# Kernel optimization log

Measured on AMD Instinct MI355X. Metric: run time of the kernel, lower is better.

## Reference

```python
import jax, jax.numpy as jnp
import numpy as np

D_MODEL = 1024
N_HEADS = 32
HEAD_DIM = D_MODEL // N_HEADS
EPS = 1e-5


def setup_inputs() -> dict:
    key = jax.random.key(0)
    ks = jax.random.split(key, 6)
    B, S = 2, 2048
    scale = 1.0 / np.sqrt(D_MODEL)
    return {
        "x": jax.random.normal(ks[0], (B, S, D_MODEL), dtype=jnp.float32),
        "Wqkv_w": jax.random.normal(ks[1], (3 * D_MODEL, D_MODEL), dtype=jnp.float32) * scale,
        "Wqkv_b": jax.random.normal(ks[2], (3 * D_MODEL,), dtype=jnp.float32) * 0.01,
        "gn_w": jnp.ones((D_MODEL,), dtype=jnp.float32),
        "gn_b": jnp.zeros((D_MODEL,), dtype=jnp.float32),
        "out_w": jax.random.normal(ks[3], (D_MODEL, D_MODEL), dtype=jnp.float32) * scale,
        "out_b": jax.random.normal(ks[4], (D_MODEL,), dtype=jnp.float32) * 0.01,
    }


def reference(x, Wqkv_w, Wqkv_b, gn_w, gn_b, out_w, out_b):
    B, S, Dm = x.shape
    H, Dh = N_HEADS, HEAD_DIM
    # QKV projection
    qkv = x @ Wqkv_w.T + Wqkv_b                      # [B,S,3*Dm]
    qkv = qkv.reshape(B, S, 3, H, Dh)
    q, k, v = qkv[:, :, 0], qkv[:, :, 1], qkv[:, :, 2]  # each [B,S,H,Dh]
    # Linear (softmax-free) attention; dropout p=0 -> identity
    a = jnp.einsum('bthd,bshd->bhts', q, k)          # [B,H,S,S]
    ctx = jnp.einsum('bhts,bshd->bthd', a, v)        # [B,S,H,Dh]
    # GroupNorm(num_groups=H, num_channels=Dm) on transposed (B, Dm, S):
    # normalizes jointly over (Dh channels, S positions) per (batch, group)
    g = ctx.transpose(0, 2, 3, 1)                    # [B,H,Dh,S]
    mean = g.mean(axis=(2, 3), keepdims=True)
    var = ((g - mean) ** 2).mean(axis=(2, 3), keepdims=True)
    gh = (g - mean) * jax.lax.rsqrt(var + EPS)
    gh = gh * gn_w.reshape(H, Dh, 1) + gn_b.reshape(H, Dh, 1)
    ctx = gh.transpose(0, 3, 1, 2).reshape(B, S, Dm)  # back to [B,S,Dm]
    return ctx @ out_w.T + out_b
```

## Files before the change

### kernel.cpp

```cpp
#include <hip/hip_runtime.h>
#include <hip/hip_bf16.h>
#include <stdint.h>

typedef unsigned short ushort_t;
typedef __attribute__((ext_vector_type(4))) float f32x4;
typedef __attribute__((ext_vector_type(8))) short short8;

#define SS 2048
#define ROWS 4096
#define EPS 1e-5f

__device__ __forceinline__ unsigned short f2bf(float f) {
  unsigned int u = __float_as_uint(f);
  u += 0x7FFF + ((u >> 16) & 1);
  return (unsigned short)(u >> 16);
}
__device__ __forceinline__ float bf2f(short s) {
  return __uint_as_float(((unsigned int)(unsigned short)s) << 16);
}

#define GLDS16(g, l)                                                        \
  __builtin_amdgcn_global_load_lds((__attribute__((address_space(1))) void*)(g), \
                                   (__attribute__((address_space(3))) void*)(l), 16, 0, 0)

__global__ __launch_bounds__(256) void f2b3_kernel(const float* __restrict__ a,
                                                   ushort_t* __restrict__ oa, int n4a,
                                                   const float* __restrict__ b,
                                                   ushort_t* __restrict__ ob, int n4b,
                                                   const float* __restrict__ c,
                                                   ushort_t* __restrict__ oc, int n4c) {
  const int stride = gridDim.x * blockDim.x;
  const int total = n4a + n4b + n4c;
  for (int i = blockIdx.x * blockDim.x + threadIdx.x; i < total; i += stride) {
    const float* src; ushort_t* dst; int idx;
    if (i < n4a)            { src = a; dst = oa; idx = i; }
    else if (i < n4a + n4b) { src = b; dst = ob; idx = i - n4a; }
    else                    { src = c; dst = oc; idx = i - n4a - n4b; }
    const float4 v = reinterpret_cast<const float4*>(src)[idx];
    ushort4 o;
    o.x = f2bf(v.x); o.y = f2bf(v.y); o.z = f2bf(v.z); o.w = f2bf(v.w);
    reinterpret_cast<ushort4*>(dst)[idx] = o;
  }
}

#define MF(d, va, vb) d = __builtin_amdgcn_mfma_f32_16x16x32_bf16(va, vb, d, 0, 0, 0)
#define LD8(p) (*reinterpret_cast<const short8*>(p))

__global__ __launch_bounds__(512, 2) void gemm1_pipe(const ushort_t* __restrict__ A,
                                                     const ushort_t* __restrict__ B,
                                                     const float* __restrict__ bias,
                                                     ushort_t* __restrict__ C) {
  __shared__ __align__(16) ushort_t lds[4 * 14336];
  const int tid = threadIdx.x;
  const int wid = tid >> 6, lane = tid & 63;
  const int bm = blockIdx.x * 256, bn = blockIdx.y * 192;
  const int wm = wid >> 2, wn = wid & 3;

  const int srow = lane >> 2;
  const int scol = ((lane & 3) ^ ((lane >> 3) & 3)) * 8;
  const int widb = (wid < 6) ? wid : 0;
  const ushort_t* gA0 = A + (size_t)(bm + wid * 16 + srow) * 1024 + scol;
  const ushort_t* gA1 = A + (size_t)(bm + (8 + wid) * 16 + srow) * 1024 + scol;
  const ushort_t* gB0 = B + (size_t)(bn + widb * 16 + srow) * 1024 + scol;
  const ushort_t* gB1 = B + (size_t)(bn + (6 + widb) * 16 + srow) * 1024 + scol;

  const int lf = lane & 15, kf = lane >> 4;
  const int flip = ((lane >> 1) & 3) << 4;
  const int aBase = (((wm * 128 + lf) * 64 + kf * 16) ^ flip) >> 1;
  const int bBase = ((((wn * 48 + lf) * 64 + kf * 16) ^ flip) >> 1) + 8192;

  f32x4 acc[8][3] = {};

#define STAGE_A(t)                                                           \
  { ushort_t* d = lds + (((t) & 3) * 14336);                                 \
    GLDS16(gA0 + (t) * 32, d + wid * 512);                                   \
    GLDS16(gA1 + (t) * 32, d + (8 + wid) * 512); }
#define STAGE_B(t)                                                           \
  if (wid < 6) { ushort_t* d = lds + (((t) & 3) * 14336) + 8192;             \
    GLDS16(gB0 + (t) * 32, d + wid * 512);                                   \
    GLDS16(gB1 + (t) * 32, d + (6 + wid) * 512); }

  STAGE_A(0) STAGE_B(0)
  STAGE_A(1) STAGE_B(1)
  STAGE_A(2) STAGE_B(2)
  if (wid < 6) { asm volatile("s_waitcnt vmcnt(8)" ::: "memory"); }
  else         { asm volatile("s_waitcnt vmcnt(4)" ::: "memory"); }
  __builtin_amdgcn_s_barrier();
  __builtin_amdgcn_sched_barrier(0);

#define K_TILE(t, DO_STAGE, VM6, VM2)                                        \
  { const ushort_t* Lb = lds + (((t) & 3) * 14336);                          \
    short8 bv0 = LD8(Lb + bBase);                                            \
    short8 bv1 = LD8(Lb + bBase + 512);                                      \
    short8 bv2 = LD8(Lb + bBase + 1024);                                     \
    short8 a0 = LD8(Lb + aBase);                                             \
    short8 a1 = LD8(Lb + aBase + 512);                                       \
    short8 a2 = LD8(Lb + aBase + 1024);                                      \
    short8 a3 = LD8(Lb + aBase + 1536);                                      \
    if (DO_STAGE) STAGE_A((t) + 3)                                           \
    __builtin_amdgcn_s_setprio(1);                                           \
    MF(acc[0][0], a0, bv0); MF(acc[1][0], a1, bv0);                          \
    MF(acc[0][1], a0, bv1); MF(acc[1][1], a1, bv1);                          \
    MF(acc[0][2], a0, bv2); MF(acc[1][2], a1, bv2);                          \
    MF(acc[2][0], a2, bv0); MF(acc[3][0], a3, bv0);                          \
    MF(acc[2][1], a2, bv1); MF(acc[3][1], a3, bv1);                          \
    MF(acc[2][2], a2, bv2); MF(acc[3][2], a3, bv2);                          \
    __builtin_amdgcn_s_setprio(0);                                           \
    a0 = LD8(Lb + aBase + 2048);                                             \
    a1 = LD8(Lb + aBase + 2560);                                             \
    a2 = LD8(Lb + aBase + 3072);                                             \
    a3 = LD8(Lb + aBase + 3584);                                             \
    if (DO_STAGE) STAGE_B((t) + 3)                                           \
    __builtin_amdgcn_s_setprio(1);                                           \
    MF(acc[4][0], a0, bv0); MF(acc[5][0], a1, bv0);                          \
    MF(acc[4][1], a0, bv1); MF(acc[5][1], a1, bv1);                          \
    MF(acc[4][2], a0, bv2); MF(acc[5][2], a1, bv2);                          \
    MF(acc[6][0], a2, bv0); MF(acc[7][0], a3, bv0);                          \
    MF(acc[6][1], a2, bv1); MF(acc[7][1], a3, bv1);                          \
    MF(acc[6][2], a2, bv2); MF(acc[7][2], a3, bv2);                          \
    __builtin_amdgcn_s_setprio(0);                                           \
    __builtin_amdgcn_sched_barrier(0);                                       \
    if (wid < 6) { asm volatile("s_waitcnt vmcnt(" #VM6 ")" ::: "memory"); } \
    else         { asm volatile("s_waitcnt vmcnt(" #VM2 ")" ::: "memory"); } \
    __builtin_amdgcn_s_barrier();                                            \
    __builtin_amdgcn_sched_barrier(0); }

#pragma unroll 1
  for (int t = 0; t < 29; ++t) K_TILE(t, 1, 8, 4)
  K_TILE(29, 0, 4, 2)
  K_TILE(30, 0, 0, 0)
  K_TILE(31, 0, 0, 0)

  const int crow = bm + wm * 128 + (lane >> 4) * 4;
  const int ccol = bn + wn * 48 + (lane & 15);
#pragma unroll
  for (int m = 0; m < 8; ++m)
#pragma unroll
    for (int n = 0; n < 3; ++n) {
      const int col = ccol + n * 16;
      const float bb = bias[col];
#pragma unroll
      for (int j = 0; j < 4; ++j)
        C[(size_t)(crow + m * 16 + j) * 3072 + col] = f2bf(acc[m][n][j] + bb);
    }
#undef K_TILE
#undef STAGE_A
#undef STAGE_B
}

__global__ __launch_bounds__(256, 2) void gemm2_pipe(const ushort_t* __restrict__ A,
                                                     const ushort_t* __restrict__ B,
                                                     const float* __restrict__ bias,
                                                     float* __restrict__ C) {
  __shared__ __align__(16) ushort_t lds[4 * 6144];
  const int tid = threadIdx.x;
  const int wid = tid >> 6, lane = tid & 63;
  const int bm = blockIdx.x * 64, bn = blockIdx.y * 128;
  const int wm = wid >> 1, wn = wid & 1;

  const int srow = lane >> 2;
  const int scol = ((lane & 3) ^ ((lane >> 3) & 3)) * 8;
  const ushort_t* gA  = A + (size_t)(bm + wid * 16 + srow) * 1024 + scol;
  const ushort_t* gB0 = B + (size_t)(bn + wid * 16 + srow) * 1024 + scol;
  const ushort_t* gB1 = B + (size_t)(bn + (4 + wid) * 16 + srow) * 1024 + scol;

  const int lf = lane & 15, kf = lane >> 4;
  const int flip = ((lane >> 1) & 3) << 4;
  const int aBase = (((wm * 32 + lf) * 64 + kf * 16) ^ flip) >> 1;
  const int bBase = ((((wn * 64 + lf) * 64 + kf * 16) ^ flip) >> 1) + 2048;

  f32x4 acc[2][4] = {};

#define STAGE2(t)                                                            \
  { ushort_t* d = lds + (((t) & 3) * 6144);                                  \
    GLDS16(gA + (t) * 32, d + wid * 512);                                    \
    GLDS16(gB0 + (t) * 32, d + 2048 + wid * 512);                            \
    GLDS16(gB1 + (t) * 32, d + 2048 + (4 + wid) * 512); }

  STAGE2(0) STAGE2(1) STAGE2(2)
  asm volatile("s_waitcnt vmcnt(6)" ::: "memory");
  __builtin_amdgcn_s_barrier();
  __builtin_amdgcn_sched_barrier(0);

#define K_TILE2(t, DO_STAGE, VM)                                             \
  { const ushort_t* Lb = lds + (((t) & 3) * 6144);                           \
    short8 bv0 = LD8(Lb + bBase);                                            \
    short8 bv1 = LD8(Lb + bBase + 512);                                      \
    short8 bv2 = LD8(Lb + bBase + 1024);                                     \
    short8 bv3 = LD8(Lb + bBase + 1536);                                     \
    short8 a0 = LD8(Lb + aBase);                                             \
    short8 a1 = LD8(Lb + aBase + 512);                                       \
    if (DO_STAGE) STAGE2((t) + 3)                                            \
    __builtin_amdgcn_s_setprio(1);                                           \
    MF(acc[0][0], a0, bv0); MF(acc[1][0], a1, bv0);                          \
    MF(acc[0][1], a0, bv1); MF(acc[1][1], a1, bv1);                          \
    MF(acc[0][2], a0, bv2); MF(acc[1][2], a1, bv2);                          \
    MF(acc[0][3], a0, bv3); MF(acc[1][3], a1, bv3);                          \
    __builtin_amdgcn_s_setprio(0);                                           \
    __builtin_amdgcn_sched_barrier(0);                                       \
    asm volatile("s_waitcnt vmcnt(" #VM ")" ::: "memory");                   \
    __builtin_amdgcn_s_barrier();                                            \
    __builtin_amdgcn_sched_barrier(0); }

#pragma unroll 1
  for (int t = 0; t < 29; ++t) K_TILE2(t, 1, 6)
  K_TILE2(29, 0, 3)
  K_TILE2(30, 0, 0)
  K_TILE2(31, 0, 0)

  const int crow = bm + wm * 32 + (lane >> 4) * 4;
  const int ccol = bn + wn * 64 + lf;
#pragma unroll
  for (int m = 0; m < 2; ++m)
#pragma unroll
    for (int n = 0; n < 4; ++n) {
      const int col = ccol + n * 16;
      const float bb = bias[col];
#pragma unroll
      for (int j = 0; j < 4; ++j)
        C[(size_t)(crow + m * 16 + j) * 1024 + col] = acc[m][n][j] + bb;
    }
#undef K_TILE2
#undef STAGE2
}

__global__ __launch_bounds__(256) void kvq_partial(const ushort_t* __restrict__ qkvb,
                                                   float* __restrict__ KVp,
                                                   float* __restrict__ Qcovp,
                                                   float* __restrict__ qsump) {
  __shared__ float qt[2048], kt[2048], vt[2048];
  const int blk = blockIdx.x;
  const int bh = blk >> 3;
  const int ch = blk & 7;
  const int b = bh >> 5, h = bh & 31;
  const int tid = threadIdx.x;
  const int r = tid >> 2, cg = (tid & 3) * 8;
  const int d = tid & 31, eg = tid >> 5;
  float kv[4] = {0.f, 0.f, 0.f, 0.f};
  float qc[4] = {0.f, 0.f, 0.f, 0.f};
  float qs = 0.f;
  for (int slab = 0; slab < 4; ++slab) {
    const ushort_t* base = qkvb +
        (size_t)(b * SS + ch * 256 + slab * 64 + r) * 3072 + h * 32 + cg;
    const short8 q8 = LD8(base);
    const short8 k8 = LD8(base + 1024);
    const short8 v8 = LD8(base + 2048);
    if (slab) __syncthreads();
#pragma unroll
    for (int i = 0; i < 8; ++i) {
      qt[r * 32 + cg + i] = bf2f(q8[i]);
      kt[r * 32 + cg + i] = bf2f(k8[i]);
      vt[r * 32 + cg + i] = bf2f(v8[i]);
    }
    __syncthreads();
#pragma unroll 4
    for (int ss = 0; ss < 64; ++ss) {
      const float vv = vt[ss * 32 + d];
      const float qd = qt[ss * 32 + d];
#pragma unroll
      for (int i = 0; i < 4; ++i) {
        kv[i] += kt[ss * 32 + eg * 4 + i] * vv;
        qc[i] += qt[ss * 32 + eg * 4 + i] * qd;
      }
    }
    if (tid < 32) {
      float s = 0.f;
      for (int ss = 0; ss < 64; ++ss) s += qt[ss * 32 + tid];
      qs += s;
    }
  }
  float* okv = KVp + ((size_t)bh * 8 + ch) * 1024 + (eg * 4) * 32 + d;
  float* oqc = Qcovp + ((size_t)bh * 8 + ch) * 1024 + (eg * 4) * 32 + d;
#pragma unroll
  for (int i = 0; i < 4; ++i) { okv[i * 32] = kv[i]; oqc[i * 32] = qc[i]; }
  if (tid < 32) qsump[((size_t)bh * 8 + ch) * 32 + tid] = qs;
}

__global__ __launch_bounds__(256) void kvq_reduce_stats(const float* __restrict__ KVp,
                                                        const float* __restrict__ Qcovp,
                                                        const float* __restrict__ qsump,
                                                        float* __restrict__ KV,
                                                        float2* __restrict__ stats) {
  __shared__ float kvs[1024], qcov[1024], qsums[32], red[16];
  const int bh = blockIdx.x;
  const int tid = threadIdx.x;
  {
    const float* kbase = KVp + (size_t)bh * 8192 + tid * 4;
    const float* qbase = Qcovp + (size_t)bh * 8192 + tid * 4;
    float4 sk = make_float4(0.f, 0.f, 0.f, 0.f);
    float4 sq = make_float4(0.f, 0.f, 0.f, 0.f);
    for (int c = 0; c < 8; ++c) {
      const float4 k4 = *(const float4*)(kbase + c * 1024);
      const float4 q4 = *(const float4*)(qbase + c * 1024);
      sk.x += k4.x; sk.y += k4.y; sk.z += k4.z; sk.w += k4.w;
      sq.x += q4.x; sq.y += q4.y; sq.z += q4.z; sq.w += q4.w;
    }
    *(float4*)&kvs[tid * 4] = sk;
    *(float4*)&qcov[tid * 4] = sq;
    *(float4*)&KV[(size_t)bh * 1024 + tid * 4] = sk;
  }
  if (tid < 32) {
    float s = 0.f;
    for (int c = 0; c < 8; ++c) s += qsump[((size_t)bh * 8 + c) * 32 + tid];
    qsums[tid] = s;
  }
  __syncthreads();
  const int d = tid & 31, ig = tid >> 5;
  float e2p = 0.f;
#pragma unroll
  for (int ii = 0; ii < 4; ++ii) {
    const int i = ig * 4 + ii;
    float t = 0.f;
#pragma unroll
    for (int j = 0; j < 32; ++j) t += qcov[i * 32 + j] * kvs[j * 32 + d];
    e2p += kvs[i * 32 + d] * t;
  }
#pragma unroll
  for (int off = 32; off > 0; off >>= 1) e2p += __shfl_down(e2p, off);
  float mp = 0.f;
  if (tid < 32) {
    float rs = 0.f;
    for (int dd = 0; dd < 32; ++dd) rs += kvs[tid * 32 + ((dd + tid) & 31)];
    mp = rs * qsums[tid];
  }
#pragma unroll
  for (int off = 32; off > 0; off >>= 1) mp += __shfl_down(mp, off);
  const int wave = tid >> 6, lane = tid & 63;
  if (lane == 0) { red[wave] = e2p; red[8 + wave] = mp; }
  __syncthreads();
  if (tid == 0) {
    const float E2 = red[0] + red[1] + red[2] + red[3];
    const float MS = red[8] + red[9] + red[10] + red[11];
    const float mean = MS * (1.f / 65536.f);
    const float var = E2 * (1.f / 65536.f) - mean * mean;
    stats[bh] = make_float2(mean, rsqrtf(var + EPS));
  }
}

__global__ __launch_bounds__(256) void ctx_norm_kernel(const ushort_t* __restrict__ qkvb,
                                                       const float* __restrict__ KV,
                                                       const float2* __restrict__ stats,
                                                       const float* __restrict__ gw,
                                                       const float* __restrict__ gb,
                                                       ushort_t* __restrict__ ghb) {
  __shared__ float kvs[1024];
  __shared__ float gws[32], gbs[32];
  const int blk = blockIdx.x;
  const int bh = blk >> 3, tt = blk & 7;
  const int b = bh >> 5, h = bh & 31;
  const int tid = threadIdx.x;
  for (int i = tid; i < 1024; i += 256) kvs[i] = KV[(size_t)bh * 1024 + i];
  if (tid < 32) { gws[tid] = gw[h * 32 + tid]; gbs[tid] = gb[h * 32 + tid]; }
  const float2 st = stats[bh];
  __syncthreads();
  const float mean = st.x, rstd = st.y;
  const int t = tt * 256 + tid;
  const ushort_t* qrow = qkvb + ((size_t)(b * SS + t)) * 3072 + h * 32;
  float q[32];
#pragma unroll
  for (int g = 0; g < 4; ++g) {
    const short8 qv = LD8(qrow + g * 8);
#pragma unroll
    for (int i = 0; i < 8; ++i) q[g * 8 + i] = bf2f(qv[i]);
  }
  float o[32];
#pragma unroll
  for (int d = 0; d < 32; ++d) o[d] = 0.f;
#pragma unroll
  for (int e = 0; e < 32; ++e) {
    const float qe = q[e];
    const float* kr = &kvs[e * 32];
#pragma unroll
    for (int d = 0; d < 32; ++d) o[d] += qe * kr[d];
  }
  ushort_t* crow = ghb + ((size_t)(b * SS + t)) * 1024 + h * 32;
#pragma unroll
  for (int g = 0; g < 4; ++g) {
    short8 ov;
#pragma unroll
    for (int i = 0; i < 8; ++i) {
      const int d = g * 8 + i;
      ov[i] = (short)f2bf((o[d] - mean) * rstd * gws[d] + gbs[d]);
    }
    *(short8*)(crow + g * 8) = ov;
  }
}

extern "C" void kernel_launch(void* const* d_in, const int* in_sizes, int n_in,
                              void* d_out, int out_size, void* d_ws, size_t ws_size,
                              hipStream_t stream) {
  const float* x  = (const float*)d_in[0];
  const float* w1 = (const float*)d_in[1];
  const float* b1 = (const float*)d_in[2];
  const float* gw = (const float*)d_in[3];
  const float* gb = (const float*)d_in[4];
  const float* w2 = (const float*)d_in[5];
  const float* b2 = (const float*)d_in[6];
  float* out = (float*)d_out;

  char* ws = (char*)d_ws;
  ushort_t* Xb    = (ushort_t*)(ws);
  float*    KVp   = (float*)(ws);
  ushort_t* W1b   = (ushort_t*)(ws + 8388608);
  float*    Qcovp = (float*)(ws + 8388608);
  ushort_t* qkvb  = (ushort_t*)(ws + 16777216);
  ushort_t* ghb   = (ushort_t*)(ws + 41943040);
  ushort_t* W2b   = (ushort_t*)(ws + 50331648);
  float*    qsump = (float*)(ws + 52428800);
  float*    KV    = (float*)(ws + 52690944);
  float2*   stats = (float2*)(ws + 52953088);

  f2b3_kernel<<<2048, 256, 0, stream>>>(x, Xb, ROWS * 1024 / 4,
                                        w1, W1b, 3072 * 1024 / 4,
                                        w2, W2b, 1024 * 1024 / 4);
  gemm1_pipe<<<dim3(16, 16), 512, 0, stream>>>(Xb, W1b, b1, qkvb);
  kvq_partial<<<512, 256, 0, stream>>>(qkvb, KVp, Qcovp, qsump);
  kvq_reduce_stats<<<64, 256, 0, stream>>>(KVp, Qcovp, qsump, KV, stats);
  ctx_norm_kernel<<<512, 256, 0, stream>>>(qkvb, KV, stats, gw, gb, ghb);
  gemm2_pipe<<<dim3(64, 8), 256, 0, stream>>>(ghb, W2b, b2, out);
}
```

Before: 90.92 us.

## Fold KV, GroupNorm affine and output weights into per-batch matrix applied to Q

The per-head context product, the GroupNorm scale and shift, and the output projection are folded algebraically into one per-batch matrix M = (W2 * scale) @ KV^T plus a folded bias. A new buildM kernel computes M and the bias. The final GEMM then reads Q directly from the qkv buffer with stride 3072 and selects the per-batch M. This removes the ctx_norm kernel, its intermediate write and read, and the W2 bf16 conversion. In exchange it adds a 2x1024x1024 matrix build and rounds the fused weights to bf16, which may change precision.

```diff
diff --git a/kernel.cpp b/kernel.cpp
--- a/kernel.cpp
+++ b/kernel.cpp
@@ -23,23 +23,19 @@
   __builtin_amdgcn_global_load_lds((__attribute__((address_space(1))) void*)(g), \
                                    (__attribute__((address_space(3))) void*)(l), 16, 0, 0)
 
-__global__ __launch_bounds__(256) void f2b3_kernel(const float* __restrict__ a,
+__global__ __launch_bounds__(256) void f2b2_kernel(const float* __restrict__ a,
                                                    ushort_t* __restrict__ oa, int n4a,
                                                    const float* __restrict__ b,
-                                                   ushort_t* __restrict__ ob, int n4b,
-                                                   const float* __restrict__ c,
-                                                   ushort_t* __restrict__ oc, int n4c) {
+                                                   ushort_t* __restrict__ ob, int n4b) {
   const int stride = gridDim.x * blockDim.x;
-  const int total = n4a + n4b + n4c;
+  const int total = n4a + n4b;
   for (int i = blockIdx.x * blockDim.x + threadIdx.x; i < total; i += stride) {
-    const float* src; ushort_t* dst; int idx;
-    if (i < n4a)            { src = a; dst = oa; idx = i; }
-    else if (i < n4a + n4b) { src = b; dst = ob; idx = i - n4a; }
-    else                    { src = c; dst = oc; idx = i - n4a - n4b; }
-    const float4 v = reinterpret_cast<const float4*>(src)[idx];
+    const float4 v = (i < n4a) ? reinterpret_cast<const float4*>(a)[i]
+                               : reinterpret_cast<const float4*>(b)[i - n4a];
     ushort4 o;
     o.x = f2bf(v.x); o.y = f2bf(v.y); o.z = f2bf(v.z); o.w = f2bf(v.w);
-    reinterpret_cast<ushort4*>(dst)[idx] = o;
+    if (i < n4a) reinterpret_cast<ushort4*>(oa)[i] = o;
+    else         reinterpret_cast<ushort4*>(ob)[i - n4a] = o;
   }
 }
 
@@ -148,7 +144,7 @@
 #undef STAGE_B
 }
 
-__global__ __launch_bounds__(256, 2) void gemm2_pipe(const ushort_t* __restrict__ A,
+__global__ __launch_bounds__(256, 2) void gemm3_pipe(const ushort_t* __restrict__ A,
                                                      const ushort_t* __restrict__ B,
                                                      const float* __restrict__ bias,
                                                      float* __restrict__ C) {
@@ -156,11 +152,12 @@
   const int tid = threadIdx.x;
   const int wid = tid >> 6, lane = tid & 63;
   const int bm = blockIdx.x * 64, bn = blockIdx.y * 128;
+  if (bm >= 2048) { B += (size_t)1024 * 1024; bias += 1024; }
   const int wm = wid >> 1, wn = wid & 1;
 
   const int srow = lane >> 2;
   const int scol = ((lane & 3) ^ ((lane >> 3) & 3)) * 8;
-  const ushort_t* gA  = A + (size_t)(bm + wid * 16 + srow) * 1024 + scol;
+  const ushort_t* gA  = A + (size_t)(bm + wid * 16 + srow) * 3072 + scol;
   const ushort_t* gB0 = B + (size_t)(bn + wid * 16 + srow) * 1024 + scol;
   const ushort_t* gB1 = B + (size_t)(bn + (4 + wid) * 16 + srow) * 1024 + scol;
 
@@ -171,18 +168,18 @@
 
   f32x4 acc[2][4] = {};
 
-#define STAGE2(t)                                                            \
+#define STAGE3(t)                                                            \
   { ushort_t* d = lds + (((t) & 3) * 6144);                                  \
     GLDS16(gA + (t) * 32, d + wid * 512);                                    \
     GLDS16(gB0 + (t) * 32, d + 2048 + wid * 512);                            \
     GLDS16(gB1 + (t) * 32, d + 2048 + (4 + wid) * 512); }
 
-  STAGE2(0) STAGE2(1) STAGE2(2)
+  STAGE3(0) STAGE3(1) STAGE3(2)
   asm volatile("s_waitcnt vmcnt(6)" ::: "memory");
   __builtin_amdgcn_s_barrier();
   __builtin_amdgcn_sched_barrier(0);
 
-#define K_TILE2(t, DO_STAGE, VM)                                             \
+#define K_TILE3(t, DO_STAGE, VM)                                             \
   { const ushort_t* Lb = lds + (((t) & 3) * 6144);                           \
     short8 bv0 = LD8(Lb + bBase);                                            \
     short8 bv1 = LD8(Lb + bBase + 512);                                      \
@@ -190,7 +187,7 @@
     short8 bv3 = LD8(Lb + bBase + 1536);                                     \
     short8 a0 = LD8(Lb + aBase);                                             \
     short8 a1 = LD8(Lb + aBase + 512);                                       \
-    if (DO_STAGE) STAGE2((t) + 3)                                            \
+    if (DO_STAGE) STAGE3((t) + 3)                                            \
     __builtin_amdgcn_s_setprio(1);                                           \
     MF(acc[0][0], a0, bv0); MF(acc[1][0], a1, bv0);                          \
     MF(acc[0][1], a0, bv1); MF(acc[1][1], a1, bv1);                          \
@@ -203,10 +200,10 @@
     __builtin_amdgcn_sched_barrier(0); }
 
 #pragma unroll 1
-  for (int t = 0; t < 29; ++t) K_TILE2(t, 1, 6)
-  K_TILE2(29, 0, 3)
-  K_TILE2(30, 0, 0)
-  K_TILE2(31, 0, 0)
+  for (int t = 0; t < 29; ++t) K_TILE3(t, 1, 6)
+  K_TILE3(29, 0, 3)
+  K_TILE3(30, 0, 0)
+  K_TILE3(31, 0, 0)
 
   const int crow = bm + wm * 32 + (lane >> 4) * 4;
   const int ccol = bn + wn * 64 + lf;
@@ -220,8 +217,8 @@
       for (int j = 0; j < 4; ++j)
         C[(size_t)(crow + m * 16 + j) * 1024 + col] = acc[m][n][j] + bb;
     }
-#undef K_TILE2
-#undef STAGE2
+#undef K_TILE3
+#undef STAGE3
 }
 
 __global__ __launch_bounds__(256) void kvq_partial(const ushort_t* __restrict__ qkvb,
@@ -337,53 +334,67 @@
   }
 }
 
-__global__ __launch_bounds__(256) void ctx_norm_kernel(const ushort_t* __restrict__ qkvb,
-                                                       const float* __restrict__ KV,
-                                                       const float2* __restrict__ stats,
-                                                       const float* __restrict__ gw,
-                                                       const float* __restrict__ gb,
-                                                       ushort_t* __restrict__ ghb) {
-  __shared__ float kvs[1024];
-  __shared__ float gws[32], gbs[32];
-  const int blk = blockIdx.x;
-  const int bh = blk >> 3, tt = blk & 7;
-  const int b = bh >> 5, h = bh & 31;
+__global__ __launch_bounds__(256) void buildM_kernel(const float* __restrict__ W2,
+                                                     const float* __restrict__ b2,
+                                                     const float* __restrict__ gw,
+                                                     const float* __restrict__ gb,
+                                                     const float2* __restrict__ stats,
+                                                     const float* __restrict__ KV,
+                                                     ushort_t* __restrict__ Ms,
+                                                     float* __restrict__ bias2) {
+  __shared__ float kvl[32 * 1032];
+  __shared__ float sS[1024], sT[1024];
+  const int b = blockIdx.y;
   const int tid = threadIdx.x;
-  for (int i = tid; i < 1024; i += 256) kvs[i] = KV[(size_t)bh * 1024 + i];
-  if (tid < 32) { gws[tid] = gw[h * 32 + tid]; gbs[tid] = gb[h * 32 + tid]; }
-  const float2 st = stats[bh];
+  for (int i = tid * 4; i < 32768; i += 1024) {
+    const float4 v = *(const float4*)&KV[(size_t)b * 32768 + i];
+    *(float4*)&kvl[i + (i >> 10) * 8] = v;
+  }
+  {
+    const int c0 = tid * 4;
+    const float2 st = stats[b * 32 + (c0 >> 5)];
+    const float4 w = *(const float4*)&gw[c0];
+    const float4 g = *(const float4*)&gb[c0];
+    sS[c0]     = st.y * w.x;  sT[c0]     = g.x - st.x * st.y * w.x;
+    sS[c0 + 1] = st.y * w.y;  sT[c0 + 1] = g.y - st.x * st.y * w.y;
+    sS[c0 + 2] = st.y * w.z;  sT[c0 + 2] = g.z - st.x * st.y * w.z;
+    sS[c0 + 3] = st.y * w.w;  sT[c0 + 3] = g.w - st.x * st.y * w.w;
+  }
   __syncthreads();
-  const float mean = st.x, rstd = st.y;
-  const int t = tt * 256 + tid;
-  const ushort_t* qrow = qkvb + ((size_t)(b * SS + t)) * 3072 + h * 32;
-  float q[32];
-#pragma unroll
-  for (int g = 0; g < 4; ++g) {
-    const short8 qv = LD8(qrow + g * 8);
-#pragma unroll
-    for (int i = 0; i < 8; ++i) q[g * 8 + i] = bf2f(qv[i]);
-  }
-  float o[32];
-#pragma unroll
-  for (int d = 0; d < 32; ++d) o[d] = 0.f;
-#pragma unroll
-  for (int e = 0; e < 32; ++e) {
-    const float qe = q[e];
-    const float* kr = &kvs[e * 32];
-#pragma unroll
-    for (int d = 0; d < 32; ++d) o[d] += qe * kr[d];
-  }
-  ushort_t* crow = ghb + ((size_t)(b * SS + t)) * 1024 + h * 32;
-#pragma unroll
-  for (int g = 0; g < 4; ++g) {
-    short8 ov;
-#pragma unroll
-    for (int i = 0; i < 8; ++i) {
-      const int d = g * 8 + i;
-      ov[i] = (short)f2bf((o[d] - mean) * rstd * gws[d] + gbs[d]);
-    }
-    *(short8*)(crow + g * 8) = ov;
-  }
+  const int n = blockIdx.x * 16 + (tid >> 4);
+  const int h0 = (tid & 15) * 2;
+  float pb = 0.f;
+#pragma unroll
+  for (int hh = 0; hh < 2; ++hh) {
+    const int h = h0 + hh;
+    float wt[32];
+#pragma unroll
+    for (int dq = 0; dq < 8; ++dq) {
+      const int c = h * 32 + dq * 4;
+      const float4 w4 = *(const float4*)&W2[(size_t)n * 1024 + c];
+      wt[dq * 4]     = w4.x * sS[c];
+      wt[dq * 4 + 1] = w4.y * sS[c + 1];
+      wt[dq * 4 + 2] = w4.z * sS[c + 2];
+      wt[dq * 4 + 3] = w4.w * sS[c + 3];
+      pb += w4.x * sT[c] + w4.y * sT[c + 1] + w4.z * sT[c + 2] + w4.w * sT[c + 3];
+    }
+    const float* kr = &kvl[h * 1032];
+    ushort_t* orow = Ms + (size_t)b * 1048576 + (size_t)n * 1024 + h * 32;
+#pragma unroll 4
+    for (int e = 0; e < 32; ++e) {
+      float dot = 0.f;
+#pragma unroll
+      for (int dq = 0; dq < 8; ++dq) {
+        const float4 k4 = *(const float4*)&kr[e * 32 + dq * 4];
+        dot += wt[dq * 4] * k4.x + wt[dq * 4 + 1] * k4.y +
+               wt[dq * 4 + 2] * k4.z + wt[dq * 4 + 3] * k4.w;
+      }
+      orow[e] = f2bf(dot);
+    }
+  }
+#pragma unroll
+  for (int off = 8; off > 0; off >>= 1) pb += __shfl_down(pb, off, 16);
+  if ((tid & 15) == 0) bias2[b * 1024 + n] = b2[n] + pb;
 }
 
 extern "C" void kernel_launch(void* const* d_in, const int* in_sizes, int n_in,
@@ -404,18 +415,16 @@
   ushort_t* W1b   = (ushort_t*)(ws + 8388608);
   float*    Qcovp = (float*)(ws + 8388608);
   ushort_t* qkvb  = (ushort_t*)(ws + 16777216);
-  ushort_t* ghb   = (ushort_t*)(ws + 41943040);
-  ushort_t* W2b   = (ushort_t*)(ws + 50331648);
+  ushort_t* Ms    = (ushort_t*)(ws + 41943040);
   float*    qsump = (float*)(ws + 52428800);
   float*    KV    = (float*)(ws + 52690944);
   float2*   stats = (float2*)(ws + 52953088);
-
-  f2b3_kernel<<<2048, 256, 0, stream>>>(x, Xb, ROWS * 1024 / 4,
-                                        w1, W1b, 3072 * 1024 / 4,
-                                        w2, W2b, 1024 * 1024 / 4);
+  float*    bias2 = (float*)(ws + 52954112);
+
+  f2b2_kernel<<<2048, 256, 0, stream>>>(x, Xb, ROWS * 1024 / 4, w1, W1b, 3072 * 1024 / 4);
   gemm1_pipe<<<dim3(16, 16), 512, 0, stream>>>(Xb, W1b, b1, qkvb);
   kvq_partial<<<512, 256, 0, stream>>>(qkvb, KVp, Qcovp, qsump);
   kvq_reduce_stats<<<64, 256, 0, stream>>>(KVp, Qcovp, qsump, KV, stats);
-  ctx_norm_kernel<<<512, 256, 0, stream>>>(qkvb, KV, stats, gw, gb, ghb);
-  gemm2_pipe<<<dim3(64, 8), 256, 0, stream>>>(ghb, W2b, b2, out);
-}
+  buildM_kernel<<<dim3(64, 2), 256, 0, stream>>>(w2, b2, gw, gb, stats, KV, Ms, bias2);
+  gemm3_pipe<<<dim3(64, 8), 256, 0, stream>>>(qkvb, Ms, bias2, out);
+}
```

Measured after the change: 109.9 us. 1.21x slower.
